# Kernel optimization log

Hardware: AMD Instinct MI355X
Metric: run time of the kernel (lower is better)

Reference implementation:

```python
import jax, jax.numpy as jnp
import numpy as np

B, T, LE = 8, 128, 128
V, VEXT = 32000, 32100
D, H, DFF, MAXLEN = 512, 8, 2048, 512


def _ln(x, g, b, eps=1e-5):
    m = jnp.mean(x, axis=-1, keepdims=True)
    v = jnp.mean((x - m) ** 2, axis=-1, keepdims=True)
    return (x - m) / jnp.sqrt(v + eps) * g + b


def _mha(q_in, k_in, v_in, in_w, in_b, out_w, out_b, mask=None):
    # torch nn.MultiheadAttention (batch_first): packed in_proj [3D, D]
    d = q_in.shape[-1]
    dh = d // H
    wq, wk, wv = in_w[:d], in_w[d:2 * d], in_w[2 * d:]
    bq, bk, bv = in_b[:d], in_b[d:2 * d], in_b[2 * d:]
    q = q_in @ wq.T + bq
    k = k_in @ wk.T + bk
    v = v_in @ wv.T + bv
    def split(x):  # [B, L, D] -> [B, H, L, dh]
        b, l, _ = x.shape
        return x.reshape(b, l, H, dh).transpose(0, 2, 1, 3)
    q, k, v = split(q), split(k), split(v)
    scores = jnp.einsum('bhqd,bhkd->bhqk', q, k) / jnp.sqrt(jnp.asarray(dh, q.dtype))
    if mask is not None:
        scores = scores + mask  # broadcast [T, T] additive mask
    attn = jax.nn.softmax(scores, axis=-1)  # [B, H, Lq, Lk]
    out = jnp.einsum('bhqk,bhkd->bhqd', attn, v)
    b, _, lq, _ = out.shape
    out = out.transpose(0, 2, 1, 3).reshape(b, lq, d)
    return out @ out_w.T + out_b, attn


def setup_inputs() -> dict:
    key = jax.random.key(0)
    ks = jax.random.split(key, 16)
    s = 0.02
    p = lambda i, shape: jax.random.normal(ks[i], shape, jnp.float32) * s
    return {
        'trg_input_ids': jax.random.randint(ks[0], (B, T), 0, V),
        'emofused': jax.random.normal(ks[1], (B, LE, D), jnp.float32),
        'src_token_ids': jax.random.randint(ks[2], (B, LE), 0, VEXT),
        'extended_vocab_size': VEXT,
        'tok_emb': p(3, (V, D)),
        'pos_emb': p(4, (MAXLEN, D)),
        'sa_in_w': p(5, (3 * D, D)), 'sa_in_b': jnp.zeros(3 * D, jnp.float32),
        'sa_out_w': p(6, (D, D)), 'sa_out_b': jnp.zeros(D, jnp.float32),
        'ca_in_w': p(7, (3 * D, D)), 'ca_in_b': jnp.zeros(3 * D, jnp.float32),
        'ca_out_w': p(8, (D, D)), 'ca_out_b': jnp.zeros(D, jnp.float32),
        'w1': p(9, (DFF, D)), 'b1': jnp.zeros(DFF, jnp.float32),
        'w2': p(10, (D, DFF)), 'b2': jnp.zeros(D, jnp.float32),
        'n1_g': jnp.ones(D, jnp.float32), 'n1_b': jnp.zeros(D, jnp.float32),
        'n2_g': jnp.ones(D, jnp.float32), 'n2_b': jnp.zeros(D, jnp.float32),
        'n3_g': jnp.ones(D, jnp.float32), 'n3_b': jnp.zeros(D, jnp.float32),
        'vp_w': p(11, (V, D)), 'vp_b': jnp.zeros(V, jnp.float32),
        'pg_w': p(12, (1, 3 * D)), 'pg_b': jnp.zeros(1, jnp.float32),
    }


def reference(trg_input_ids, emofused, src_token_ids, extended_vocab_size,
              tok_emb, pos_emb, sa_in_w, sa_in_b, sa_out_w, sa_out_b,
              ca_in_w, ca_in_b, ca_out_w, ca_out_b, w1, b1, w2, b2,
              n1_g, n1_b, n2_g, n2_b, n3_g, n3_b, vp_w, vp_b, pg_w, pg_b):
    t = trg_input_ids.shape[1]
    emb = tok_emb[trg_input_ids]                      # [B, T, D]
    x = emb + pos_emb[:t][None]
    # causal additive mask [T, T]
    idx = jnp.arange(t)
    mask = jnp.where(idx[None, :] > idx[:, None], jnp.asarray(-1e9, x.dtype), 0.0)
    # pre-norm self-attn
    h = _ln(x, n1_g, n1_b)
    sa, _ = _mha(h, h, h, sa_in_w, sa_in_b, sa_out_w, sa_out_b, mask)
    x = x + sa
    # pre-norm cross-attn (emofused is sole KV)
    h = _ln(x, n2_g, n2_b)
    ca, ca_attn = _mha(h, emofused, emofused, ca_in_w, ca_in_b, ca_out_w, ca_out_b)
    x = x + ca
    # FFN
    h = _ln(x, n3_g, n3_b)
    x = x + (jax.nn.relu(h @ w1.T + b1) @ w2.T + b2)
    hidden = x
    attn_avg = ca_attn.mean(axis=1)                   # [B, T, LE]
    ctx = jnp.einsum('btl,bld->btd', attn_avg, emofused)
    Pgen = jax.nn.softmax(hidden @ vp_w.T + vp_b, axis=-1)  # [B, T, V]
    gate_in = jnp.concatenate([hidden, ctx, emb], axis=-1)
    p_mix = jax.nn.sigmoid(gate_in @ pg_w.T + pg_b)   # [B, T, 1]
    vext = int(extended_vocab_size)
    def scat(aw, src):  # aw [T, LE], src [LE] -> [T, Vext]
        return jnp.zeros((aw.shape[0], vext), aw.dtype).at[:, src].add(aw)
    Pcopy = jax.vmap(scat)(attn_avg, src_token_ids)   # [B, T, Vext]
    Pgen_ext = jnp.pad(Pgen, ((0, 0), (0, 0), (0, vext - Pgen.shape[-1])))
    Pw = p_mix * Pgen_ext + (1.0 - p_mix) * Pcopy
    return Pw, Pgen_ext, Pcopy, p_mix, hidden, attn_avg, ctx
```

## Files before the change

kernel.cpp:

```cpp
#include <hip/hip_runtime.h>
#include <hip/hip_bf16.h>

using bf16   = __hip_bfloat16;
using bf16x8 = __attribute__((ext_vector_type(8))) __bf16;
using f32x4  = __attribute__((ext_vector_type(4))) float;
using short8 = __attribute__((ext_vector_type(8))) short;

__device__ __forceinline__ unsigned short f2b(float x) {
  union { bf16 b; unsigned short u; } t; t.b = __float2bfloat16(x); return t.u;
}
__device__ __forceinline__ float b2f(unsigned short u) {
  union { unsigned int i; float f; } t; t.i = ((unsigned int)u) << 16; return t.f;
}

typedef __attribute__((address_space(1))) const unsigned int* gas1_t;
typedef __attribute__((address_space(3))) unsigned int* las3_t;
__device__ __forceinline__ void gload16(const void* g, void* l) {
  __builtin_amdgcn_global_load_lds((gas1_t)g, (las3_t)l, 16, 0, 0);
}

__global__ __launch_bounds__(256) void k_cast(const float* __restrict__ s, bf16* __restrict__ d, int n4) {
  int i = blockIdx.x * 256 + threadIdx.x;
  int str = gridDim.x * 256;
  for (; i < n4; i += str) {
    float4 v = ((const float4*)s)[i];
    ushort4 u; u.x = f2b(v.x); u.y = f2b(v.y); u.z = f2b(v.z); u.w = f2b(v.w);
    ((ushort4*)d)[i] = u;
  }
}

__global__ __launch_bounds__(256) void k_cast_multi(
    const float* __restrict__ s0, bf16* __restrict__ d0,
    const float* __restrict__ s1, bf16* __restrict__ d1,
    const float* __restrict__ s2, bf16* __restrict__ d2,
    const float* __restrict__ s3, bf16* __restrict__ d3,
    const float* __restrict__ s4, bf16* __restrict__ d4,
    const float* __restrict__ s5, bf16* __restrict__ d5,
    const float* __restrict__ s6, bf16* __restrict__ d6) {
  int i = blockIdx.x * 256 + threadIdx.x;
  const float* s; bf16* d; int off;
  if      (i <  196608) { s = s0; d = d0; off = i; }
  else if (i <  262144) { s = s1; d = d1; off = i - 196608; }
  else if (i <  458752) { s = s2; d = d2; off = i - 262144; }
  else if (i <  524288) { s = s3; d = d3; off = i - 458752; }
  else if (i <  786432) { s = s4; d = d4; off = i - 524288; }
  else if (i < 1048576) { s = s5; d = d5; off = i - 786432; }
  else                  { s = s6; d = d6; off = i - 1048576; }
  float4 v = ((const float4*)s)[off];
  ushort4 u; u.x = f2b(v.x); u.y = f2b(v.y); u.z = f2b(v.z); u.w = f2b(v.w);
  ((ushort4*)d)[off] = u;
}

__global__ __launch_bounds__(256) void k_embed_ln(const int* __restrict__ ids, const float* __restrict__ tok,
                                                  const float* __restrict__ pos, const float* __restrict__ g,
                                                  const float* __restrict__ bb, float* __restrict__ x,
                                                  float* __restrict__ emb, bf16* __restrict__ o) {
  int wid = threadIdx.x >> 6, lane = threadIdx.x & 63;
  int row = blockIdx.x * 4 + wid;
  int tt = row & 127;
  int id = ids[row];
  int d = lane * 8;
  float4 e0 = *(const float4*)&tok[(size_t)id * 512 + d];
  float4 e1 = *(const float4*)&tok[(size_t)id * 512 + d + 4];
  float4 p0 = *(const float4*)&pos[(size_t)tt * 512 + d];
  float4 p1 = *(const float4*)&pos[(size_t)tt * 512 + d + 4];
  *(float4*)&emb[(size_t)row * 512 + d]     = e0;
  *(float4*)&emb[(size_t)row * 512 + d + 4] = e1;
  float4 v0; v0.x = e0.x + p0.x; v0.y = e0.y + p0.y; v0.z = e0.z + p0.z; v0.w = e0.w + p0.w;
  float4 v1; v1.x = e1.x + p1.x; v1.y = e1.y + p1.y; v1.z = e1.z + p1.z; v1.w = e1.w + p1.w;
  *(float4*)&x[(size_t)row * 512 + d]     = v0;
  *(float4*)&x[(size_t)row * 512 + d + 4] = v1;
  float s = v0.x + v0.y + v0.z + v0.w + v1.x + v1.y + v1.z + v1.w;
  float q = v0.x*v0.x + v0.y*v0.y + v0.z*v0.z + v0.w*v0.w
          + v1.x*v1.x + v1.y*v1.y + v1.z*v1.z + v1.w*v1.w;
#pragma unroll
  for (int t = 32; t; t >>= 1) { s += __shfl_xor(s, t); q += __shfl_xor(q, t); }
  float mean = s * (1.f / 512.f);
  float var  = q * (1.f / 512.f) - mean * mean;
  float rstd = rsqrtf(var + 1e-5f);
  float4 g0 = *(const float4*)&g[d],  g1 = *(const float4*)&g[d + 4];
  float4 b0 = *(const float4*)&bb[d], b1 = *(const float4*)&bb[d + 4];
  short8 pk;
  pk[0] = (short)f2b((v0.x - mean) * rstd * g0.x + b0.x);
  pk[1] = (short)f2b((v0.y - mean) * rstd * g0.y + b0.y);
  pk[2] = (short)f2b((v0.z - mean) * rstd * g0.z + b0.z);
  pk[3] = (short)f2b((v0.w - mean) * rstd * g0.w + b0.w);
  pk[4] = (short)f2b((v1.x - mean) * rstd * g1.x + b1.x);
  pk[5] = (short)f2b((v1.y - mean) * rstd * g1.y + b1.y);
  pk[6] = (short)f2b((v1.z - mean) * rstd * g1.z + b1.z);
  pk[7] = (short)f2b((v1.w - mean) * rstd * g1.w + b1.w);
  *(short8*)&o[(size_t)row * 512 + d] = pk;
}

__global__ __launch_bounds__(256) void k_ln(const float* __restrict__ x, const float* __restrict__ g,
                                            const float* __restrict__ bb, bf16* __restrict__ o) {
  int wid = threadIdx.x >> 6, lane = threadIdx.x & 63;
  int row = blockIdx.x * 4 + wid;
  const float* xr = x + (size_t)row * 512;
  int d = lane * 8;
  float4 v0 = *(const float4*)&xr[d];
  float4 v1 = *(const float4*)&xr[d + 4];
  float s = v0.x + v0.y + v0.z + v0.w + v1.x + v1.y + v1.z + v1.w;
  float q = v0.x*v0.x + v0.y*v0.y + v0.z*v0.z + v0.w*v0.w
          + v1.x*v1.x + v1.y*v1.y + v1.z*v1.z + v1.w*v1.w;
#pragma unroll
  for (int t = 32; t; t >>= 1) { s += __shfl_xor(s, t); q += __shfl_xor(q, t); }
  float mean = s * (1.f / 512.f);
  float var  = q * (1.f / 512.f) - mean * mean;
  float rstd = rsqrtf(var + 1e-5f);
  float4 g0 = *(const float4*)&g[d],  g1 = *(const float4*)&g[d + 4];
  float4 b0 = *(const float4*)&bb[d], b1 = *(const float4*)&bb[d + 4];
  short8 pk;
  pk[0] = (short)f2b((v0.x - mean) * rstd * g0.x + b0.x);
  pk[1] = (short)f2b((v0.y - mean) * rstd * g0.y + b0.y);
  pk[2] = (short)f2b((v0.z - mean) * rstd * g0.z + b0.z);
  pk[3] = (short)f2b((v0.w - mean) * rstd * g0.w + b0.w);
  pk[4] = (short)f2b((v1.x - mean) * rstd * g1.x + b1.x);
  pk[5] = (short)f2b((v1.y - mean) * rstd * g1.y + b1.y);
  pk[6] = (short)f2b((v1.z - mean) * rstd * g1.z + b1.z);
  pk[7] = (short)f2b((v1.w - mean) * rstd * g1.w + b1.w);
  *(short8*)&o[(size_t)row * 512 + d] = pk;
}

template<int RELU, int RESID, int OUTBF, int SWZ, int HID>
__global__ __launch_bounds__(256) void k_gemm(const bf16* __restrict__ A, const bf16* __restrict__ Wt,
                                              const float* __restrict__ bias, const float* __restrict__ resid,
                                              void* __restrict__ Cout, bf16* __restrict__ hidb,
                                              int K, int ldc) {
  __shared__ __align__(16) float cst[32 * 132];
  bf16* Al = (bf16*)cst;
  bf16* Bl = (bf16*)cst + 4096;
  int t = threadIdx.x;
  int lane = t & 63;
  int wid = t >> 6;
  int wr = wid >> 1, wc = wid & 1;
  int trow, tcol;
  if (SWZ) {
    int bid = blockIdx.y * gridDim.x + blockIdx.x;
    int swz = (bid & 7) * 250 + (bid >> 3);
    trow = (swz & 7) * 128;
    tcol = (swz >> 3) * 128;
  } else {
    trow = blockIdx.y * 128; tcol = blockIdx.x * 128;
  }
  f32x4 acc[4][4] = {};
  const int kh = (lane >> 4) * 8;
  const int rl = lane & 15;
  const int srow = lane >> 2;
  const int scol = (lane & 3) * 8;
  for (int kt = 0; kt < K; kt += 32) {
    __syncthreads();
#pragma unroll
    for (int s = 0; s < 2; ++s) {
      int c = wid * 2 + s;
      int row = c * 16 + srow;
      gload16(A  + (size_t)(trow + row) * K + kt + scol, &Al[c * 512]);
      gload16(Wt + (size_t)(tcol + row) * K + kt + scol, &Bl[c * 512]);
    }
    __syncthreads();
    bf16x8 af[4], bg[4];
#pragma unroll
    for (int m = 0; m < 4; ++m) af[m] = *(const bf16x8*)&Al[(wr * 64 + m * 16 + rl) * 32 + kh];
#pragma unroll
    for (int n = 0; n < 4; ++n) bg[n] = *(const bf16x8*)&Bl[(wc * 64 + n * 16 + rl) * 32 + kh];
#pragma unroll
    for (int m = 0; m < 4; ++m)
#pragma unroll
      for (int n = 0; n < 4; ++n)
        acc[m][n] = __builtin_amdgcn_mfma_f32_16x16x32_bf16(af[m], bg[n], acc[m][n], 0, 0, 0);
  }
  const int s   = t >> 3;
  const int seg = (t & 7) * 16;
  float bv[16];
#pragma unroll
  for (int q = 0; q < 16; q += 4) *(float4*)&bv[q] = *(const float4*)&bias[tcol + seg + q];
#pragma unroll
  for (int m = 0; m < 4; ++m) {
    __syncthreads();
#pragma unroll
    for (int n = 0; n < 4; ++n) {
      int col = wc * 64 + n * 16 + rl;
#pragma unroll
      for (int j = 0; j < 4; ++j) {
        int sr = wr * 16 + (lane >> 4) * 4 + j;
        cst[sr * 132 + col] = acc[m][n][j];
      }
    }
    __syncthreads();
    int grow = trow + m * 16 + (s < 16 ? s : 48 + s);
    size_t base = (size_t)grow * ldc + tcol + seg;
    float v[16];
#pragma unroll
    for (int q = 0; q < 16; q += 4) {
      float4 f = *(float4*)&cst[s * 132 + seg + q];
      v[q] = f.x; v[q+1] = f.y; v[q+2] = f.z; v[q+3] = f.w;
    }
    if (RESID) {
#pragma unroll
      for (int q = 0; q < 16; q += 4) {
        float4 r = *(const float4*)&resid[base + q];
        v[q] += r.x; v[q+1] += r.y; v[q+2] += r.z; v[q+3] += r.w;
      }
    }
#pragma unroll
    for (int q = 0; q < 16; ++q) {
      float val = v[q] + bv[q];
      if (RELU) val = fmaxf(val, 0.f);
      v[q] = val;
    }
    if (RESID) {
    }
    if (OUTBF) {
      short8 p0, p1;
#pragma unroll
      for (int q = 0; q < 8; ++q) { p0[q] = (short)f2b(v[q]); p1[q] = (short)f2b(v[8 + q]); }
      *(short8*)&((bf16*)Cout)[base]     = p0;
      *(short8*)&((bf16*)Cout)[base + 8] = p1;
    } else {
#pragma unroll
      for (int q = 0; q < 16; q += 4) {
        float4 o; o.x = v[q]; o.y = v[q+1]; o.z = v[q+2]; o.w = v[q+3];
        *(float4*)&((float*)Cout)[base + q] = o;
      }
      if (HID) {
        short8 p0, p1;
#pragma unroll
        for (int q = 0; q < 8; ++q) { p0[q] = (short)f2b(v[q]); p1[q] = (short)f2b(v[8 + q]); }
        *(short8*)&hidb[base]     = p0;
        *(short8*)&hidb[base + 8] = p1;
      }
    }
  }
}

template<int MASK, int WPROB>
__global__ __launch_bounds__(256) void k_attn(const float* __restrict__ Qb, int qs,
                                              const float* __restrict__ Kb, int ks,
                                              const float* __restrict__ Vb, int vs,
                                              float* __restrict__ probs, bf16* __restrict__ Ob, int os) {
  __shared__ float KV[128][68];
  __shared__ float Sc[32][132];
  int t = threadIdx.x;
  int bh = blockIdx.x; int b = bh >> 3, h = bh & 7;
  int rb = blockIdx.y * 32;
  int r = t >> 3, sub = t & 7;
  const float* Kp = Kb + (size_t)(b * 128) * ks + h * 64;
  const float* Vp = Vb + (size_t)(b * 128) * vs + h * 64;
  const float* Qp = Qb + (size_t)(b * 128 + rb + r) * qs + h * 64;
  float4 q[16];
#pragma unroll
  for (int i = 0; i < 16; ++i) q[i] = *(const float4*)&Qp[i * 4];
  for (int i = 0; i < 32; ++i) { int u = t + i * 256; int rr = u >> 6, dd = u & 63; KV[rr][dd] = Kp[(size_t)rr * ks + dd]; }
  __syncthreads();
  float sc[16];
#pragma unroll
  for (int i = 0; i < 16; ++i) {
    int c = sub + i * 8;
    float a = 0.f;
#pragma unroll
    for (int d4 = 0; d4 < 16; ++d4) {
      float4 k4 = *(const float4*)&KV[c][d4 * 4];
      a += q[d4].x * k4.x + q[d4].y * k4.y + q[d4].z * k4.z + q[d4].w * k4.w;
    }
    a *= 0.125f;
    if (MASK && c > rb + r) a -= 1e9f;
    sc[i] = a;
  }
  float mx = -1e30f;
#pragma unroll
  for (int i = 0; i < 16; ++i) mx = fmaxf(mx, sc[i]);
  mx = fmaxf(mx, __shfl_xor(mx, 1)); mx = fmaxf(mx, __shfl_xor(mx, 2)); mx = fmaxf(mx, __shfl_xor(mx, 4));
  float sm = 0.f;
#pragma unroll
  for (int i = 0; i < 16; ++i) { sc[i] = __expf(sc[i] - mx); sm += sc[i]; }
  sm += __shfl_xor(sm, 1); sm += __shfl_xor(sm, 2); sm += __shfl_xor(sm, 4);
  float inv = 1.f / sm;
#pragma unroll
  for (int i = 0; i < 16; ++i) {
    float p = sc[i] * inv;
    Sc[r][sub + i * 8] = p;
    if (WPROB) probs[(((size_t)(b * 8 + h) * 128) + rb + r) * 128 + sub + i * 8] = p;
  }
  __syncthreads();
  for (int i = 0; i < 32; ++i) { int u = t + i * 256; int rr = u >> 6, dd = u & 63; KV[rr][dd] = Vp[(size_t)rr * vs + dd]; }
  __syncthreads();
  int dg = sub;
  float4 o0 = {0,0,0,0}, o1 = {0,0,0,0};
  for (int j = 0; j < 128; ++j) {
    float p = Sc[r][j];
    float4 va = *(const float4*)&KV[j][dg * 8];
    float4 vb = *(const float4*)&KV[j][dg * 8 + 4];
    o0.x += p * va.x; o0.y += p * va.y; o0.z += p * va.z; o0.w += p * va.w;
    o1.x += p * vb.x; o1.y += p * vb.y; o1.z += p * vb.z; o1.w += p * vb.w;
  }
  short8 pk;
  pk[0] = (short)f2b(o0.x); pk[1] = (short)f2b(o0.y); pk[2] = (short)f2b(o0.z); pk[3] = (short)f2b(o0.w);
  pk[4] = (short)f2b(o1.x); pk[5] = (short)f2b(o1.y); pk[6] = (short)f2b(o1.z); pk[7] = (short)f2b(o1.w);
  *(short8*)&Ob[(size_t)(b * 128 + rb + r) * os + h * 64 + dg * 8] = pk;
}

__global__ __launch_bounds__(256) void k_ctx2(const float* __restrict__ abuf, const float* __restrict__ emo,
                                              float* __restrict__ aavg, float* __restrict__ ctx) {
  __shared__ float aw[8][132];
  int b = blockIdx.x, rb = blockIdx.y * 8;
  int t = threadIdx.x;
  for (int i = t; i < 1024; i += 256) {
    int r = i >> 7, l = i & 127;
    float s = 0.f;
#pragma unroll
    for (int h = 0; h < 8; ++h) s += abuf[(((size_t)(b * 8 + h) * 128) + rb + r) * 128 + l];
    s *= 0.125f;
    aw[r][l] = s;
    aavg[(size_t)(b * 128 + rb + r) * 128 + l] = s;
  }
  __syncthreads();
  int d = t * 2;
  float2 acc[8] = {};
  for (int l = 0; l < 128; ++l) {
    float2 e = *(const float2*)&emo[(size_t)(b * 128 + l) * 512 + d];
#pragma unroll
    for (int r = 0; r < 8; ++r) { acc[r].x += aw[r][l] * e.x; acc[r].y += aw[r][l] * e.y; }
  }
#pragma unroll
  for (int r = 0; r < 8; ++r) *(float2*)&ctx[(size_t)(b * 128 + rb + r) * 512 + d] = acc[r];
}

__global__ __launch_bounds__(256) void k_gate(const float* __restrict__ hid, const float* __restrict__ ctx,
                                              const float* __restrict__ emb, const float* __restrict__ pgw,
                                              const float* __restrict__ pgb, float* __restrict__ pmix) {
  int wid = threadIdx.x >> 6, lane = threadIdx.x & 63;
  int row = blockIdx.x * 4 + wid;
  float s = 0.f;
#pragma unroll
  for (int i = 0; i < 8; ++i) {
    int d = lane + i * 64;
    s = fmaf(hid[(size_t)row * 512 + d], pgw[d], s);
    s = fmaf(ctx[(size_t)row * 512 + d], pgw[512 + d], s);
    s = fmaf(emb[(size_t)row * 512 + d], pgw[1024 + d], s);
  }
#pragma unroll
  for (int t = 32; t; t >>= 1) s += __shfl_xor(s, t);
  if (lane == 0) pmix[row] = 1.f / (1.f + __expf(-(s + pgb[0])));
}

__global__ __launch_bounds__(256) void k_softmax_final(
    const bf16* __restrict__ lg, const float* __restrict__ pmix,
    float* __restrict__ pgen, float* __restrict__ pw, float* __restrict__ pcopy) {
  __shared__ float red[4];
  int row = blockIdx.x;
  int t = threadIdx.x, lane = t & 63, wid = t >> 6;
  const bf16* L = lg + (size_t)row * 32000;
  float s = 0.f;
  for (int i = t; i < 4000; i += 256) {
    short8 v = *(const short8*)(L + i * 8);
#pragma unroll
    for (int c = 0; c < 8; ++c) s += __expf(b2f((unsigned short)v[c]));
  }
#pragma unroll
  for (int o = 32; o; o >>= 1) s += __shfl_xor(s, o);
  if (lane == 0) red[wid] = s;
  __syncthreads();
  s = red[0] + red[1] + red[2] + red[3];
  float inv = 1.f / s;
  float pm = pmix[row];
  float* pgen_r  = pgen  + (size_t)row * 32100;
  float* pw_r    = pw    + (size_t)row * 32100;
  float* pcopy_r = pcopy + (size_t)row * 32100;
  float4 z = {0.f, 0.f, 0.f, 0.f};
  for (int i = t; i < 4000; i += 256) {
    short8 v = *(const short8*)(L + i * 8);
    float p[8];
#pragma unroll
    for (int c = 0; c < 8; ++c) p[c] = __expf(b2f((unsigned short)v[c])) * inv;
    float4 a0 = {p[0], p[1], p[2], p[3]};
    float4 a1 = {p[4], p[5], p[6], p[7]};
    *(float4*)&pgen_r[i * 8]     = a0;
    *(float4*)&pgen_r[i * 8 + 4] = a1;
    float4 w0 = {pm * p[0], pm * p[1], pm * p[2], pm * p[3]};
    float4 w1 = {pm * p[4], pm * p[5], pm * p[6], pm * p[7]};
    *(float4*)&pw_r[i * 8]     = w0;
    *(float4*)&pw_r[i * 8 + 4] = w1;
    *(float4*)&pcopy_r[i * 8]     = z;
    *(float4*)&pcopy_r[i * 8 + 4] = z;
  }
  if (t < 25) {
    int c = 32000 + t * 4;
    *(float4*)&pgen_r[c] = z; *(float4*)&pw_r[c] = z; *(float4*)&pcopy_r[c] = z;
  }
}

__global__ __launch_bounds__(256) void k_scatter(const int* __restrict__ src, const float* __restrict__ aavg,
                                                 const float* __restrict__ pmix, float* __restrict__ pw,
                                                 float* __restrict__ pcopy) {
  int tid = blockIdx.x * 256 + threadIdx.x;
  int row = tid >> 4, slot = tid & 15;
  int b = row >> 7;
  float qg = 1.f - pmix[row];
#pragma unroll
  for (int i = 0; i < 8; ++i) {
    int l = slot * 8 + i;
    int c = src[b * 128 + l];
    float w = aavg[(size_t)row * 128 + l];
    atomicAdd(&pcopy[(size_t)row * 32100 + c], w);
    atomicAdd(&pw[(size_t)row * 32100 + c], qg * w);
  }
}

extern "C" void kernel_launch(void* const* d_in, const int* in_sizes, int n_in,
                              void* d_out, int out_size, void* d_ws, size_t ws_size,
                              hipStream_t stream) {
  const int*   ids      = (const int*)d_in[0];
  const float* emo      = (const float*)d_in[1];
  const int*   src      = (const int*)d_in[2];
  const float* tok      = (const float*)d_in[4];
  const float* pos      = (const float*)d_in[5];
  const float* sa_in_w  = (const float*)d_in[6];
  const float* sa_in_b  = (const float*)d_in[7];
  const float* sa_out_w = (const float*)d_in[8];
  const float* sa_out_b = (const float*)d_in[9];
  const float* ca_in_w  = (const float*)d_in[10];
  const float* ca_in_b  = (const float*)d_in[11];
  const float* ca_out_w = (const float*)d_in[12];
  const float* ca_out_b = (const float*)d_in[13];
  const float* w1       = (const float*)d_in[14];
  const float* b1       = (const float*)d_in[15];
  const float* w2       = (const float*)d_in[16];
  const float* b2       = (const float*)d_in[17];
  const float* n1g      = (const float*)d_in[18];
  const float* n1b      = (const float*)d_in[19];
  const float* n2g      = (const float*)d_in[20];
  const float* n2b      = (const float*)d_in[21];
  const float* n3g      = (const float*)d_in[22];
  const float* n3b      = (const float*)d_in[23];
  const float* vpw      = (const float*)d_in[24];
  const float* vpb      = (const float*)d_in[25];
  const float* pgw      = (const float*)d_in[26];
  const float* pgb      = (const float*)d_in[27];
  (void)in_sizes; (void)n_in; (void)out_size; (void)ws_size;

  constexpr size_t NR = 1024;
  float* out     = (float*)d_out;
  float* o_pw    = out;
  float* o_pgen  = out + NR * 32100;
  float* o_pcopy = out + 2 * NR * 32100;
  float* o_pmix  = out + 3 * NR * 32100;
  float* o_hid   = o_pmix + NR;
  float* o_aavg  = o_hid + NR * 512;
  float* o_ctx   = o_aavg + NR * 128;

  char* wp = (char*)d_ws;
  size_t off = 0;
  auto alloc = [&](size_t bytes) { char* r = wp + off; off += (bytes + 255) & ~(size_t)255; return r; };
  bf16*  sa_in_bf  = (bf16*)alloc(3 * 512 * 512 * 2);
  bf16*  sa_out_bf = (bf16*)alloc(512 * 512 * 2);
  bf16*  ca_in_bf  = (bf16*)alloc(3 * 512 * 512 * 2);
  bf16*  ca_out_bf = (bf16*)alloc(512 * 512 * 2);
  bf16*  w1_bf     = (bf16*)alloc(2048 * 512 * 2);
  bf16*  w2_bf     = (bf16*)alloc(2048 * 512 * 2);
  bf16*  vp_bf     = (bf16*)alloc((size_t)32000 * 512 * 2);
  bf16*  emo_bf    = (bf16*)alloc(8 * 128 * 512 * 2);
  float* x         = (float*)alloc(1024 * 512 * 4);
  float* embf      = (float*)alloc(1024 * 512 * 4);
  bf16*  hbf       = (bf16*)alloc(1024 * 512 * 2);
  float* qkv       = (float*)alloc(1024 * 1536 * 4);
  bf16*  aout_bf   = (bf16*)alloc(1024 * 512 * 2);
  float* qca       = (float*)alloc(1024 * 512 * 4);
  float* kvca      = (float*)alloc(1024 * 1024 * 4);
  float* abuf      = (float*)alloc((size_t)8 * 8 * 128 * 128 * 4);
  bf16*  f1bf      = (bf16*)alloc(1024 * 2048 * 2);
  bf16*  hid_bf    = (bf16*)alloc(1024 * 512 * 2);
  bf16*  logits_bf = (bf16*)alloc((size_t)1024 * 32000 * 2);

  k_cast_multi<<<4608, 256, 0, stream>>>(sa_in_w, sa_in_bf, sa_out_w, sa_out_bf,
                                         ca_in_w, ca_in_bf, ca_out_w, ca_out_bf,
                                         w1, w1_bf, w2, w2_bf, emo, emo_bf);
  k_cast<<<2048, 256, 0, stream>>>(vpw, vp_bf, 4096000);

  k_embed_ln<<<256, 256, 0, stream>>>(ids, tok, pos, n1g, n1b, x, embf, hbf);

  k_gemm<0,0,0,0,0><<<dim3(12, 8), 256, 0, stream>>>(hbf, sa_in_bf, sa_in_b, nullptr, qkv, nullptr, 512, 1536);
  k_attn<1,0><<<dim3(64, 4), 256, 0, stream>>>(qkv, 1536, qkv + 512, 1536, qkv + 1024, 1536,
                                               nullptr, aout_bf, 512);
  k_gemm<0,1,0,0,0><<<dim3(4, 8), 256, 0, stream>>>(aout_bf, sa_out_bf, sa_out_b, x, x, nullptr, 512, 512);

  k_ln<<<256, 256, 0, stream>>>(x, n2g, n2b, hbf);
  k_gemm<0,0,0,0,0><<<dim3(4, 8), 256, 0, stream>>>(hbf, ca_in_bf, ca_in_b, nullptr, qca, nullptr, 512, 512);
  k_gemm<0,0,0,0,0><<<dim3(8, 8), 256, 0, stream>>>(emo_bf, ca_in_bf + 512 * 512, ca_in_b + 512,
                                                    nullptr, kvca, nullptr, 512, 1024);
  k_attn<0,1><<<dim3(64, 4), 256, 0, stream>>>(qca, 512, kvca, 1024, kvca + 512, 1024,
                                               abuf, aout_bf, 512);
  k_ctx2<<<dim3(8, 16), 256, 0, stream>>>(abuf, emo, o_aavg, o_ctx);
  k_gemm<0,1,0,0,0><<<dim3(4, 8), 256, 0, stream>>>(aout_bf, ca_out_bf, ca_out_b, x, x, nullptr, 512, 512);

  k_ln<<<256, 256, 0, stream>>>(x, n3g, n3b, hbf);
  k_gemm<1,0,1,0,0><<<dim3(16, 8), 256, 0, stream>>>(hbf, w1_bf, b1, nullptr, f1bf, nullptr, 512, 2048);
  k_gemm<0,1,0,0,1><<<dim3(4, 8), 256, 0, stream>>>(f1bf, w2_bf, b2, x, o_hid, hid_bf, 2048, 512);

  k_gate<<<256, 256, 0, stream>>>(o_hid, o_ctx, embf, pgw, pgb, o_pmix);

  k_gemm<0,0,1,1,0><<<dim3(8, 250), 256, 0, stream>>>(hid_bf, vp_bf, vpb, nullptr, logits_bf, nullptr, 512, 32000);
  k_softmax_final<<<1024, 256, 0, stream>>>(logits_bf, o_pmix, o_pgen, o_pw, o_pcopy);
  k_scatter<<<64, 256, 0, stream>>>(src, o_aavg, o_pmix, o_pw, o_pcopy);
}
```

Before: 444.6 us.

## Fuse softmax row-sum into vocab GEMM epilogue and merge casts and gate

The vocab projection GEMM epilogue now computes exp of its bf16 logits and atomically adds per-row sums. This removes the first full pass over the logits in the softmax kernel. The gate dot-product is folded into the softmax kernel, the two cast kernels are merged into one grid-stride kernel that also zeroes the row-sum buffer, and the large output writes use nontemporal stores. The cost is per-row atomics in the GEMM epilogue and extra exp work there, plus summation order that is no longer deterministic.

```diff
diff --git a/kernel.cpp b/kernel.cpp
--- a/kernel.cpp
+++ b/kernel.cpp
@@ -12,6 +12,10 @@
 __device__ __forceinline__ float b2f(unsigned short u) {
   union { unsigned int i; float f; } t; t.i = ((unsigned int)u) << 16; return t.f;
 }
+__device__ __forceinline__ void ntst4(float* p, float a, float b, float c, float d) {
+  f32x4 v = {a, b, c, d};
+  __builtin_nontemporal_store(v, (f32x4*)p);
+}
 
 typedef __attribute__((address_space(1))) const unsigned int* gas1_t;
 typedef __attribute__((address_space(3))) unsigned int* las3_t;
@@ -19,36 +23,41 @@
   __builtin_amdgcn_global_load_lds((gas1_t)g, (las3_t)l, 16, 0, 0);
 }
 
-__global__ __launch_bounds__(256) void k_cast(const float* __restrict__ s, bf16* __restrict__ d, int n4) {
-  int i = blockIdx.x * 256 + threadIdx.x;
-  int str = gridDim.x * 256;
-  for (; i < n4; i += str) {
-    float4 v = ((const float4*)s)[i];
-    ushort4 u; u.x = f2b(v.x); u.y = f2b(v.y); u.z = f2b(v.z); u.w = f2b(v.w);
-    ((ushort4*)d)[i] = u;
-  }
-}
-
-__global__ __launch_bounds__(256) void k_cast_multi(
+__global__ __launch_bounds__(256) void k_cast_all(
+    const float* __restrict__ vpsrc, bf16* __restrict__ vpdst,
     const float* __restrict__ s0, bf16* __restrict__ d0,
     const float* __restrict__ s1, bf16* __restrict__ d1,
     const float* __restrict__ s2, bf16* __restrict__ d2,
     const float* __restrict__ s3, bf16* __restrict__ d3,
     const float* __restrict__ s4, bf16* __restrict__ d4,
     const float* __restrict__ s5, bf16* __restrict__ d5,
-    const float* __restrict__ s6, bf16* __restrict__ d6) {
+    const float* __restrict__ s6, bf16* __restrict__ d6,
+    float* __restrict__ rowsum) {
   int i = blockIdx.x * 256 + threadIdx.x;
-  const float* s; bf16* d; int off;
-  if      (i <  196608) { s = s0; d = d0; off = i; }
-  else if (i <  262144) { s = s1; d = d1; off = i - 196608; }
-  else if (i <  458752) { s = s2; d = d2; off = i - 262144; }
-  else if (i <  524288) { s = s3; d = d3; off = i - 458752; }
-  else if (i <  786432) { s = s4; d = d4; off = i - 524288; }
-  else if (i < 1048576) { s = s5; d = d5; off = i - 786432; }
-  else                  { s = s6; d = d6; off = i - 1048576; }
-  float4 v = ((const float4*)s)[off];
-  ushort4 u; u.x = f2b(v.x); u.y = f2b(v.y); u.z = f2b(v.z); u.w = f2b(v.w);
-  ((ushort4*)d)[off] = u;
+  int str = gridDim.x * 256;
+  for (; i < 5275904; i += str) {
+    if (i < 4096000) {
+      float4 v = ((const float4*)vpsrc)[i];
+      ushort4 u; u.x = f2b(v.x); u.y = f2b(v.y); u.z = f2b(v.z); u.w = f2b(v.w);
+      ((ushort4*)vpdst)[i] = u;
+    } else if (i < 5275648) {
+      int j = i - 4096000;
+      const float* s; bf16* d; int off;
+      if      (j <  196608) { s = s0; d = d0; off = j; }
+      else if (j <  262144) { s = s1; d = d1; off = j - 196608; }
+      else if (j <  458752) { s = s2; d = d2; off = j - 262144; }
+      else if (j <  524288) { s = s3; d = d3; off = j - 458752; }
+      else if (j <  786432) { s = s4; d = d4; off = j - 524288; }
+      else if (j < 1048576) { s = s5; d = d5; off = j - 786432; }
+      else                  { s = s6; d = d6; off = j - 1048576; }
+      float4 v = ((const float4*)s)[off];
+      ushort4 u; u.x = f2b(v.x); u.y = f2b(v.y); u.z = f2b(v.z); u.w = f2b(v.w);
+      ((ushort4*)d)[off] = u;
+    } else {
+      float4 z = {0.f, 0.f, 0.f, 0.f};
+      ((float4*)rowsum)[i - 5275648] = z;
+    }
+  }
 }
 
 __global__ __launch_bounds__(256) void k_embed_ln(const int* __restrict__ ids, const float* __restrict__ tok,
@@ -122,11 +131,11 @@
   *(short8*)&o[(size_t)row * 512 + d] = pk;
 }
 
-template<int RELU, int RESID, int OUTBF, int SWZ, int HID>
+template<int RELU, int RESID, int OUTBF, int SWZ, int HID, int EXPS>
 __global__ __launch_bounds__(256) void k_gemm(const bf16* __restrict__ A, const bf16* __restrict__ Wt,
                                               const float* __restrict__ bias, const float* __restrict__ resid,
                                               void* __restrict__ Cout, bf16* __restrict__ hidb,
-                                              int K, int ldc) {
+                                              float* __restrict__ rowsum, int K, int ldc) {
   __shared__ __align__(16) float cst[32 * 132];
   bf16* Al = (bf16*)cst;
   bf16* Bl = (bf16*)cst + 4096;
@@ -208,14 +217,20 @@
       if (RELU) val = fmaxf(val, 0.f);
       v[q] = val;
     }
-    if (RESID) {
-    }
     if (OUTBF) {
       short8 p0, p1;
 #pragma unroll
       for (int q = 0; q < 8; ++q) { p0[q] = (short)f2b(v[q]); p1[q] = (short)f2b(v[8 + q]); }
       *(short8*)&((bf16*)Cout)[base]     = p0;
       *(short8*)&((bf16*)Cout)[base + 8] = p1;
+      if (EXPS) {
+        float e = 0.f;
+#pragma unroll
+        for (int q = 0; q < 8; ++q)
+          e += __expf(b2f((unsigned short)p0[q])) + __expf(b2f((unsigned short)p1[q]));
+        e += __shfl_xor(e, 1); e += __shfl_xor(e, 2); e += __shfl_xor(e, 4);
+        if ((t & 7) == 0) atomicAdd(&rowsum[grow], e);
+      }
     } else {
 #pragma unroll
       for (int q = 0; q < 16; q += 4) {
@@ -325,67 +340,55 @@
   for (int r = 0; r < 8; ++r) *(float2*)&ctx[(size_t)(b * 128 + rb + r) * 512 + d] = acc[r];
 }
 
-__global__ __launch_bounds__(256) void k_gate(const float* __restrict__ hid, const float* __restrict__ ctx,
-                                              const float* __restrict__ emb, const float* __restrict__ pgw,
-                                              const float* __restrict__ pgb, float* __restrict__ pmix) {
-  int wid = threadIdx.x >> 6, lane = threadIdx.x & 63;
-  int row = blockIdx.x * 4 + wid;
-  float s = 0.f;
-#pragma unroll
-  for (int i = 0; i < 8; ++i) {
-    int d = lane + i * 64;
-    s = fmaf(hid[(size_t)row * 512 + d], pgw[d], s);
-    s = fmaf(ctx[(size_t)row * 512 + d], pgw[512 + d], s);
-    s = fmaf(emb[(size_t)row * 512 + d], pgw[1024 + d], s);
-  }
-#pragma unroll
-  for (int t = 32; t; t >>= 1) s += __shfl_xor(s, t);
-  if (lane == 0) pmix[row] = 1.f / (1.f + __expf(-(s + pgb[0])));
-}
-
 __global__ __launch_bounds__(256) void k_softmax_final(
-    const bf16* __restrict__ lg, const float* __restrict__ pmix,
-    float* __restrict__ pgen, float* __restrict__ pw, float* __restrict__ pcopy) {
+    const bf16* __restrict__ lg, const float* __restrict__ rowsum,
+    const float* __restrict__ hid, const float* __restrict__ ctx, const float* __restrict__ emb,
+    const float* __restrict__ pgw, const float* __restrict__ pgb,
+    float* __restrict__ pmix_out, float* __restrict__ pgen, float* __restrict__ pw,
+    float* __restrict__ pcopy) {
   __shared__ float red[4];
   int row = blockIdx.x;
   int t = threadIdx.x, lane = t & 63, wid = t >> 6;
-  const bf16* L = lg + (size_t)row * 32000;
-  float s = 0.f;
-  for (int i = t; i < 4000; i += 256) {
-    short8 v = *(const short8*)(L + i * 8);
-#pragma unroll
-    for (int c = 0; c < 8; ++c) s += __expf(b2f((unsigned short)v[c]));
+  float s;
+  {
+    int d = t * 2;
+    float2 h2 = *(const float2*)&hid[(size_t)row * 512 + d];
+    float2 c2 = *(const float2*)&ctx[(size_t)row * 512 + d];
+    float2 e2 = *(const float2*)&emb[(size_t)row * 512 + d];
+    float2 g0 = *(const float2*)&pgw[d];
+    float2 g1 = *(const float2*)&pgw[512 + d];
+    float2 g2 = *(const float2*)&pgw[1024 + d];
+    s = h2.x*g0.x + h2.y*g0.y + c2.x*g1.x + c2.y*g1.y + e2.x*g2.x + e2.y*g2.y;
   }
 #pragma unroll
   for (int o = 32; o; o >>= 1) s += __shfl_xor(s, o);
   if (lane == 0) red[wid] = s;
   __syncthreads();
   s = red[0] + red[1] + red[2] + red[3];
-  float inv = 1.f / s;
-  float pm = pmix[row];
+  float pm = 1.f / (1.f + __expf(-(s + pgb[0])));
+  if (t == 0) pmix_out[row] = pm;
+  float inv = 1.f / rowsum[row];
+  const bf16* L = lg + (size_t)row * 32000;
   float* pgen_r  = pgen  + (size_t)row * 32100;
   float* pw_r    = pw    + (size_t)row * 32100;
   float* pcopy_r = pcopy + (size_t)row * 32100;
-  float4 z = {0.f, 0.f, 0.f, 0.f};
   for (int i = t; i < 4000; i += 256) {
     short8 v = *(const short8*)(L + i * 8);
     float p[8];
 #pragma unroll
     for (int c = 0; c < 8; ++c) p[c] = __expf(b2f((unsigned short)v[c])) * inv;
-    float4 a0 = {p[0], p[1], p[2], p[3]};
-    float4 a1 = {p[4], p[5], p[6], p[7]};
-    *(float4*)&pgen_r[i * 8]     = a0;
-    *(float4*)&pgen_r[i * 8 + 4] = a1;
-    float4 w0 = {pm * p[0], pm * p[1], pm * p[2], pm * p[3]};
-    float4 w1 = {pm * p[4], pm * p[5], pm * p[6], pm * p[7]};
-    *(float4*)&pw_r[i * 8]     = w0;
-    *(float4*)&pw_r[i * 8 + 4] = w1;
-    *(float4*)&pcopy_r[i * 8]     = z;
-    *(float4*)&pcopy_r[i * 8 + 4] = z;
+    ntst4(&pgen_r[i * 8],     p[0], p[1], p[2], p[3]);
+    ntst4(&pgen_r[i * 8 + 4], p[4], p[5], p[6], p[7]);
+    ntst4(&pw_r[i * 8],     pm * p[0], pm * p[1], pm * p[2], pm * p[3]);
+    ntst4(&pw_r[i * 8 + 4], pm * p[4], pm * p[5], pm * p[6], pm * p[7]);
+    ntst4(&pcopy_r[i * 8],     0.f, 0.f, 0.f, 0.f);
+    ntst4(&pcopy_r[i * 8 + 4], 0.f, 0.f, 0.f, 0.f);
   }
   if (t < 25) {
     int c = 32000 + t * 4;
-    *(float4*)&pgen_r[c] = z; *(float4*)&pw_r[c] = z; *(float4*)&pcopy_r[c] = z;
+    ntst4(&pgen_r[c], 0.f, 0.f, 0.f, 0.f);
+    ntst4(&pw_r[c],   0.f, 0.f, 0.f, 0.f);
+    ntst4(&pcopy_r[c], 0.f, 0.f, 0.f, 0.f);
   }
 }
 
@@ -470,35 +473,37 @@
   bf16*  f1bf      = (bf16*)alloc(1024 * 2048 * 2);
   bf16*  hid_bf    = (bf16*)alloc(1024 * 512 * 2);
   bf16*  logits_bf = (bf16*)alloc((size_t)1024 * 32000 * 2);
-
-  k_cast_multi<<<4608, 256, 0, stream>>>(sa_in_w, sa_in_bf, sa_out_w, sa_out_bf,
-                                         ca_in_w, ca_in_bf, ca_out_w, ca_out_bf,
-                                         w1, w1_bf, w2, w2_bf, emo, emo_bf);
-  k_cast<<<2048, 256, 0, stream>>>(vpw, vp_bf, 4096000);
+  float* rowsum    = (float*)alloc(1024 * 4);
+
+  k_cast_all<<<4608, 256, 0, stream>>>(vpw, vp_bf,
+                                       sa_in_w, sa_in_bf, sa_out_w, sa_out_bf,
+                                       ca_in_w, ca_in_bf, ca_out_w, ca_out_bf,
+                                       w1, w1_bf, w2, w2_bf, emo, emo_bf, rowsum);
 
   k_embed_ln<<<256, 256, 0, stream>>>(ids, tok, pos, n1g, n1b, x, embf, hbf);
 
-  k_gemm<0,0,0,0,0><<<dim3(12, 8), 256, 0, stream>>>(hbf, sa_in_bf, sa_in_b, nullptr, qkv, nullptr, 512, 1536);
+  k_gemm<0,0,0,0,0,0><<<dim3(12, 8), 256, 0, stream>>>(hbf, sa_in_bf, sa_in_b, nullptr, qkv, nullptr, nullptr, 512, 1536);
   k_attn<1,0><<<dim3(64, 4), 256, 0, stream>>>(qkv, 1536, qkv + 512, 1536, qkv + 1024, 1536,
                                                nullptr, aout_bf, 512);
-  k_gemm<0,1,0,0,0><<<dim3(4, 8), 256, 0, stream>>>(aout_bf, sa_out_bf, sa_out_b, x, x, nullptr, 512, 512);
+  k_gemm<0,1,0,0,0,0><<<dim3(4, 8), 256, 0, stream>>>(aout_bf, sa_out_bf, sa_out_b, x, x, nullptr, nullptr, 512, 512);
 
   k_ln<<<256, 256, 0, stream>>>(x, n2g, n2b, hbf);
-  k_gemm<0,0,0,0,0><<<dim3(4, 8), 256, 0, stream>>>(hbf, ca_in_bf, ca_in_b, nullptr, qca, nullptr, 512, 512);
-  k_gemm<0,0,0,0,0><<<dim3(8, 8), 256, 0, stream>>>(emo_bf, ca_in_bf + 512 * 512, ca_in_b + 512,
-                                                    nullptr, kvca, nullptr, 512, 1024);
+  k_gemm<0,0,0,0,0,0><<<dim3(4, 8), 256, 0, stream>>>(hbf, ca_in_bf, ca_in_b, nullptr, qca, nullptr, nullptr, 512, 512);
+  k_gemm<0,0,0,0,0,0><<<dim3(8, 8), 256, 0, stream>>>(emo_bf, ca_in_bf + 512 * 512, ca_in_b + 512,
+                                                      nullptr, kvca, nullptr, nullptr, 512, 1024);
   k_attn<0,1><<<dim3(64, 4), 256, 0, stream>>>(qca, 512, kvca, 1024, kvca + 512, 1024,
                                                abuf, aout_bf, 512);
   k_ctx2<<<dim3(8, 16), 256, 0, stream>>>(abuf, emo, o_aavg, o_ctx);
-  k_gemm<0,1,0,0,0><<<dim3(4, 8), 256, 0, stream>>>(aout_bf, ca_out_bf, ca_out_b, x, x, nullptr, 512, 512);
+  k_gemm<0,1,0,0,0,0><<<dim3(4, 8), 256, 0, stream>>>(aout_bf, ca_out_bf, ca_out_b, x, x, nullptr, nullptr, 512, 512);
 
   k_ln<<<256, 256, 0, stream>>>(x, n3g, n3b, hbf);
-  k_gemm<1,0,1,0,0><<<dim3(16, 8), 256, 0, stream>>>(hbf, w1_bf, b1, nullptr, f1bf, nullptr, 512, 2048);
-  k_gemm<0,1,0,0,1><<<dim3(4, 8), 256, 0, stream>>>(f1bf, w2_bf, b2, x, o_hid, hid_bf, 2048, 512);
-
-  k_gate<<<256, 256, 0, stream>>>(o_hid, o_ctx, embf, pgw, pgb, o_pmix);
-
-  k_gemm<0,0,1,1,0><<<dim3(8, 250), 256, 0, stream>>>(hid_bf, vp_bf, vpb, nullptr, logits_bf, nullptr, 512, 32000);
-  k_softmax_final<<<1024, 256, 0, stream>>>(logits_bf, o_pmix, o_pgen, o_pw, o_pcopy);
+  k_gemm<1,0,1,0,0,0><<<dim3(16, 8), 256, 0, stream>>>(hbf, w1_bf, b1, nullptr, f1bf, nullptr, nullptr, 512, 2048);
+  k_gemm<0,1,0,0,1,0><<<dim3(4, 8), 256, 0, stream>>>(f1bf, w2_bf, b2, x, o_hid, hid_bf, nullptr, 2048, 512);
+
+  k_gemm<0,0,1,1,0,1><<<dim3(8, 250), 256, 0, stream>>>(hid_bf, vp_bf, vpb, nullptr, logits_bf, nullptr, rowsum, 512, 32000);
+
+  k_softmax_final<<<1024, 256, 0, stream>>>(logits_bf, rowsum, o_hid, o_ctx, embf, pgw, pgb,
+                                            o_pmix, o_pgen, o_pw, o_pcopy);
+
   k_scatter<<<64, 256, 0, stream>>>(src, o_aavg, o_pmix, o_pw, o_pcopy);
 }
```

After: 464.3 us. +4.4%, slower.
